# Kernel tuning notes

Hardware: AMD Instinct MI355X
Metric: run time of the kernel (lower is better)

The kernel has to match this reference:

```python
import jax, jax.numpy as jnp
import numpy as np

KH, KW, STRIDE, PAD, DIL = 3, 3, 1, 1, 1


def setup_inputs() -> dict:
    key = jax.random.key(0)
    ks = jax.random.split(key, 4)
    B, C, H, W, O = 4, 256, 64, 64, 256
    K = KH * KW
    x = jax.random.normal(ks[0], (B, C, H, W), jnp.float32)
    # offset/mask conv params (original inits to zero; use small random so offsets are non-trivial)
    w_om = jax.random.normal(ks[1], (3 * K, C, KH, KW), jnp.float32) * 0.01
    b_om = jnp.zeros((3 * K,), jnp.float32)
    # main weight: kaiming_uniform_(a=1) -> gain = sqrt(2/(1+1^2)) = 1, bound = sqrt(3)/sqrt(fan_in)
    fan_in = C * K
    bound = float(np.sqrt(3.0) / np.sqrt(fan_in))
    weight = jax.random.uniform(ks[2], (O, C, KH, KW), jnp.float32, -bound, bound)
    bias = jnp.zeros((O,), jnp.float32)
    return {"x": x, "w_om": w_om, "b_om": b_om, "weight": weight, "bias": bias}


def _deform_conv2d(x, offset, mask, weight, bias):
    # torchvision.ops.deform_conv2d semantics, deformable_groups=1, stride=1, pad=1, dil=1
    B, C, H, W = x.shape
    K = KH * KW
    # torchvision offset layout: per-tap interleaved (y, x) pairs along channel dim
    off_y = offset[:, 0::2]  # [B, K, H, W]
    off_x = offset[:, 1::2]  # [B, K, H, W]
    ky = (jnp.repeat(jnp.arange(KH), KW) * DIL).astype(x.dtype)  # [K]
    kx = (jnp.tile(jnp.arange(KW), KH) * DIL).astype(x.dtype)    # [K]
    base_y = (jnp.arange(H) * STRIDE - PAD).astype(x.dtype)
    base_x = (jnp.arange(W) * STRIDE - PAD).astype(x.dtype)
    py = base_y[None, None, :, None] + ky[None, :, None, None] + off_y  # [B,K,H,W]
    px = base_x[None, None, None, :] + kx[None, :, None, None] + off_x  # [B,K,H,W]
    y0 = jnp.floor(py)
    x0 = jnp.floor(px)
    ly = py - y0
    lx = px - x0
    y0i = y0.astype(jnp.int32)
    x0i = x0.astype(jnp.int32)
    x_flat = x.reshape(B, C, H * W)

    def gather(yy, xx):
        # zero-padded gather of one bilinear corner -> [B, C, K, H, W]
        valid = ((yy >= 0) & (yy < H) & (xx >= 0) & (xx < W)).astype(x.dtype)
        idx = (jnp.clip(yy, 0, H - 1) * W + jnp.clip(xx, 0, W - 1)).reshape(B, -1)
        g = jax.vmap(lambda xf, i: jnp.take(xf, i, axis=1))(x_flat, idx)
        return g.reshape(B, C, K, H, W) * valid.reshape(B, 1, K, H, W)

    w00 = ((1 - ly) * (1 - lx))[:, None]
    w01 = ((1 - ly) * lx)[:, None]
    w10 = (ly * (1 - lx))[:, None]
    w11 = (ly * lx)[:, None]
    val = (gather(y0i, x0i) * w00 + gather(y0i, x0i + 1) * w01
           + gather(y0i + 1, x0i) * w10 + gather(y0i + 1, x0i + 1) * w11)
    cols = val * mask[:, None]  # modulated columns [B,C,K,H,W]
    out = jnp.einsum('bckhw,ock->bohw', cols, weight.reshape(weight.shape[0], C, K))
    return out + bias[None, :, None, None]


def reference(x, w_om, b_om, weight, bias):
    om = jax.lax.conv_general_dilated(
        x, w_om, (STRIDE, STRIDE), ((PAD, PAD), (PAD, PAD)),
        rhs_dilation=(DIL, DIL), dimension_numbers=('NCHW', 'OIHW', 'NCHW'),
    ) + b_om[None, :, None, None]
    K = KH * KW
    o1, o2, m = om[:, :K], om[:, K:2 * K], om[:, 2 * K:]
    offset = jnp.concatenate([o1, o2], axis=1)  # [B, 2K, H, W]
    mask = jax.nn.sigmoid(m)                    # [B, K, H, W]
    return _deform_conv2d(x, offset, mask, weight, bias)
```

## Files before the change

kernel.cpp:

```cpp
#include <hip/hip_runtime.h>
#include <stdint.h>

#define B_ 4
#define C_ 256
#define H_ 64
#define W_ 64
#define O_ 256
#define K_ 9
#define CK 2304
#define HW 4096
#define NTOT 16384

typedef __bf16 bf16x8 __attribute__((ext_vector_type(8)));
typedef __bf16 bf16x4 __attribute__((ext_vector_type(4)));
typedef float f32x4 __attribute__((ext_vector_type(4)));
typedef float f32x2 __attribute__((ext_vector_type(2)));
typedef f32x2 __attribute__((aligned(4))) f32x2u;

__device__ __forceinline__ uint16_t f2bf(float f) {
  uint32_t u = __builtin_bit_cast(uint32_t, f);
  return (uint16_t)((u + 0x7FFFu + ((u >> 16) & 1u)) >> 16);
}

__device__ __forceinline__ uint32_t pk_bf16(float a, float b) {
  uint16_t lo = __builtin_bit_cast(uint16_t, (__bf16)a);
  uint16_t hi = __builtin_bit_cast(uint16_t, (__bf16)b);
  return (uint32_t)lo | ((uint32_t)hi << 16);
}

__global__ void kA_prep(const float* __restrict__ weight, const float* __restrict__ w_om,
                        const float* __restrict__ x, uint16_t* __restrict__ wb,
                        uint16_t* __restrict__ womb, uint16_t* __restrict__ xT) {
  int bx = blockIdx.x;
  int t = threadIdx.x;
  if (bx < 2304) {
    int idx = bx * 256 + t;
    int o = idx / CK;
    int rem = idx - o * CK;
    int k = rem >> 8, c = rem & 255;
    wb[idx] = f2bf(weight[(o * C_ + c) * K_ + k]);
  } else if (bx < 2592) {
    int idx = (bx - 2304) * 256 + t;
    int j = idx / CK;
    int ck = idx - j * CK;
    int k = ck >> 8, c = ck & 255;
    womb[idx] = (j < 27) ? f2bf(w_om[(j * 256 + c) * 9 + k]) : (uint16_t)0;
  } else {
    int bxl = bx - 2592;
    int ct = bxl & 3;
    int hwt = (bxl >> 2) & 63;
    int b = bxl >> 8;
    int l = t & 63;
    int cq = t >> 6;

    __shared__ __align__(16) uint16_t tile[64 * 72];

    const float* xb = x + ((b * 256 + ct * 64) * HW) + hwt * 64;
#pragma unroll
    for (int i = 0; i < 16; ++i) {
      int c = cq * 16 + i;
      tile[l * 72 + c] = f2bf(xb[c * HW + l]);
    }
    __syncthreads();

    int hw = t >> 2;
    int c8 = (t & 3) * 8;
    uint16_t* dst = xT + ((size_t)b << 20) + (size_t)(hwt * 64 + hw) * 256 + ct * 64;
    *(uint4*)&dst[c8] = *(const uint4*)&tile[hw * 72 + c8];
    *(uint4*)&dst[c8 + 32] = *(const uint4*)&tile[hw * 72 + c8 + 32];
  }
}

__device__ __forceinline__ void write_om(float v, int j, int n, const float* __restrict__ b_om,
                                         float* __restrict__ pypxmk) {
  if (j >= 27) return;
  float s = v + b_om[j];
  int b = n >> 12, hw = n & 4095;
  int h = hw >> 6, w = hw & 63;
  if (j < 18) {
    int k = j >> 1;
    int off = (b * 9 + k) * HW + hw;
    if ((j & 1) == 0)
      pypxmk[off] = (float)(h - 1 + k / 3) + s;
    else
      pypxmk[147456 + off] = (float)(w - 1 + k % 3) + s;
  } else {
    int k = j - 18;
    pypxmk[294912 + (b * 9 + k) * HW + hw] = 1.f / (1.f + __expf(-s));
  }
}

__global__ void k1_mfma(const uint16_t* __restrict__ womb, const uint16_t* __restrict__ xT,
                        const float* __restrict__ b_om, float* __restrict__ pypxmk) {
  int nt = blockIdx.x;
  int t = threadIdx.x;
  int lane = t & 63;
  int wid = t >> 6;
  int lr = lane & 15, q = lane >> 4;
  int n = nt * 64 + wid * 16 + lr;
  int b = n >> 12;
  int hw = n & 4095;
  int y = hw >> 6, xx = hw & 63;
  const uint16_t* xb = xT + ((size_t)b << 20);
  const uint16_t* zrow = womb + 31 * CK;

  f32x4 acc0 = {0.f, 0.f, 0.f, 0.f};
  f32x4 acc1 = {0.f, 0.f, 0.f, 0.f};

#pragma unroll
  for (int k = 0; k < 9; ++k) {
    int dy = k / 3, dx = k - dy * 3;
    int ny = y + dy - 1, nx = xx + dx - 1;
    bool valid = ((unsigned)ny < 64u) && ((unsigned)nx < 64u);
    int row = (min(max(ny, 0), 63) << 6) + min(max(nx, 0), 63);
    const uint16_t* bp = valid ? (xb + row * 256 + q * 8) : (zrow + q * 8);
    const uint16_t* ap = womb + lr * CK + k * 256 + q * 8;
#pragma unroll
    for (int kt = 0; kt < 8; ++kt) {
      int c0 = kt * 32;
      bf16x8 bF = *(const bf16x8*)&bp[c0];
      bf16x8 aF0 = *(const bf16x8*)&ap[c0];
      bf16x8 aF1 = *(const bf16x8*)&ap[16 * CK + c0];
      acc0 = __builtin_amdgcn_mfma_f32_16x16x32_bf16(aF0, bF, acc0, 0, 0, 0);
      acc1 = __builtin_amdgcn_mfma_f32_16x16x32_bf16(aF1, bF, acc1, 0, 0, 0);
    }
  }

#pragma unroll
  for (int r = 0; r < 4; ++r) {
    write_om(acc0[r], q * 4 + r, n, b_om, pypxmk);
    write_om(acc1[r], 16 + q * 4 + r, n, b_om, pypxmk);
  }
}


struct GatherState {
  float wa0[4], wb0[4], wa1[4], wb1[4];
  bf16x4 r00[4], r01[4], r10[4], r11[4];
};

__device__ __forceinline__ void gather_issue(GatherState& S, const uint16_t* __restrict__ xb,
                                             const float* __restrict__ pyA,
                                             const float* __restrict__ pxA,
                                             const float* __restrict__ mkA,
                                             int b, int kg, int n0, int rbase, int lane) {
#pragma unroll
  for (int j = 0; j < 4; ++j) {
    int nrow = rbase + j;
    int poff = (b * 9 + kg) * HW + ((n0 + nrow) & 4095);
    float py = pyA[poff];
    float px = pxA[poff];
    float mk = mkA[poff];
    float fy0 = floorf(py), fx0 = floorf(px);
    float ly = py - fy0, lx = px - fx0;
    int y0 = (int)fy0, x0 = (int)fx0;
    bool vy0 = ((unsigned)y0 < 64u), vy1 = ((unsigned)(y0 + 1) < 64u);
    bool vx0 = ((unsigned)x0 < 64u), vx1 = ((unsigned)(x0 + 1) < 64u);
    float w00 = (vy0 && vx0) ? (1.f - ly) * (1.f - lx) * mk : 0.f;
    float w01 = (vy0 && vx1) ? (1.f - ly) * lx * mk : 0.f;
    float w10 = (vy1 && vx0) ? ly * (1.f - lx) * mk : 0.f;
    float w11 = (vy1 && vx1) ? ly * lx * mk : 0.f;
    bool sel0 = (x0 >= 63);
    bool sel1 = (x0 >= 0);
    S.wa0[j] = (sel0 ? 0.f : w00) + (sel1 ? 0.f : w01);
    S.wb0[j] = (sel0 ? w00 : 0.f) + (sel1 ? w01 : 0.f);
    S.wa1[j] = (sel0 ? 0.f : w10) + (sel1 ? 0.f : w11);
    S.wb1[j] = (sel0 ? w10 : 0.f) + (sel1 ? w11 : 0.f);
    int bx0 = min(max(x0, 0), 62);
    int a0 = min(max(y0, 0), 63) * 64 + bx0;
    int a1 = min(max(y0 + 1, 0), 63) * 64 + bx0;
    S.r00[j] = *(const bf16x4*)&xb[a0 * 256 + lane * 4];
    S.r01[j] = *(const bf16x4*)&xb[a0 * 256 + 256 + lane * 4];
    S.r10[j] = *(const bf16x4*)&xb[a1 * 256 + lane * 4];
    S.r11[j] = *(const bf16x4*)&xb[a1 * 256 + 256 + lane * 4];
  }
}

__device__ __forceinline__ void gather_finish(const GatherState& S, uint16_t* bslab,
                                              int rbase, int lane) {
#pragma unroll
  for (int j = 0; j < 4; ++j) {
    int nrow = rbase + j;
    float v[4];
#pragma unroll
    for (int i = 0; i < 4; ++i)
      v[i] = S.wa0[j] * (float)S.r00[j][i] + S.wb0[j] * (float)S.r01[j][i] +
             S.wa1[j] * (float)S.r10[j][i] + S.wb1[j] * (float)S.r11[j][i];
    uint2 pk;
    pk.x = pk_bf16(v[0], v[1]);
    pk.y = pk_bf16(v[2], v[3]);
    int chunk = lane >> 1;
    int chs = (chunk & 24) | ((chunk & 7) ^ (nrow & 7));
    *(uint2*)&bslab[nrow * 256 + chs * 8 + (lane & 1) * 4] = pk;
  }
}

__device__ __forceinline__ void stageA(const uint16_t* __restrict__ wb, uint16_t* asbuf,
                                       int kbase, int t) {
#pragma unroll
  for (int i = 0; i < 4; ++i) {
    int rr = i * 64 + (t >> 3);
    const uint16_t* src = wb + rr * CK + kbase + (((t & 7) ^ (rr & 7)) << 3);
    __builtin_amdgcn_global_load_lds(
        (const __attribute__((address_space(1))) uint32_t*)src,
        (__attribute__((address_space(3))) uint32_t*)&asbuf[i * 4096 + t * 8], 16, 0, 0);
  }
}

__device__ __forceinline__ void mma_step(const uint16_t* AsP, const uint16_t* BsP,
                                         f32x4 acc[4][2], int wm, int wn, int lr, int q,
                                         int kt2) {
#pragma unroll
  for (int kc = 0; kc < 2; ++kc) {
    bf16x8 aF[4], bF[2];
#pragma unroll
    for (int i = 0; i < 4; ++i) {
      int row = wm * 64 + i * 16 + lr;
      aF[i] = *(const bf16x8*)&AsP[row * 64 + (((kc * 4 + q) ^ (row & 7)) << 3)];
    }
#pragma unroll
    for (int j = 0; j < 2; ++j) {
      int row = wn * 32 + j * 16 + lr;
      int kidx = kt2 * 8 + kc * 4 + q;
      int chs = (kidx & 24) | ((kidx & 7) ^ (row & 7));
      bF[j] = *(const bf16x8*)&BsP[row * 256 + chs * 8];
    }
#pragma unroll
    for (int i = 0; i < 4; ++i)
#pragma unroll
      for (int j = 0; j < 2; ++j)
        acc[i][j] = __builtin_amdgcn_mfma_f32_16x16x32_bf16(aF[i], bF[j], acc[i][j], 0, 0, 0);
  }
}

__global__ __launch_bounds__(512, 2) void k23_fused(const uint16_t* __restrict__ wb,
                                                    const uint16_t* __restrict__ xT,
                                                    const float* __restrict__ pypxmk,
                                                    const float* __restrict__ bias,
                                                    float* __restrict__ out) {
  __shared__ __align__(16) uint16_t As[2][16384];
  __shared__ __align__(16) uint16_t Bs[2][16384];

  int t = threadIdx.x;
  int lane = t & 63;
  int wid = __builtin_amdgcn_readfirstlane(t >> 6);
  int lr = lane & 15, q = lane >> 4;
  int wm = wid >> 1, wn = wid & 1;
  int bx = blockIdx.x;
  int swz = (bx & 7) * 32 + (bx >> 3);
  int n0 = swz * 64;
  int b = n0 >> 12;
  int hw0 = n0 & 4095;
  const uint16_t* xb = xT + ((size_t)b << 20);
  const float* pyA = pypxmk;
  const float* pxA = pypxmk + 147456;
  const float* mkA = pypxmk + 294912;

  f32x4 acc[4][2];
  const f32x4 zero = {0.f, 0.f, 0.f, 0.f};
#pragma unroll
  for (int i = 0; i < 4; ++i)
#pragma unroll
    for (int j = 0; j < 2; ++j) acc[i][j] = zero;

  GatherState S;
  int wrow = wid * 8;

  gather_issue(S, xb, pyA, pxA, mkA, b, 0, n0, wrow, lane);
  gather_finish(S, Bs[0], wrow, lane);
  gather_issue(S, xb, pyA, pxA, mkA, b, 0, n0, wrow + 4, lane);
  gather_finish(S, Bs[0], wrow + 4, lane);
  stageA(wb, As[0], 0, t);
  __syncthreads();

  for (int k = 0; k < 9; ++k) {
    uint16_t* BsC = Bs[k & 1];
    uint16_t* BsN = Bs[(k & 1) ^ 1];
    for (int kt2 = 0; kt2 < 4; ++kt2) {
      if (!(k == 8 && kt2 == 3)) {
        int kb2 = (kt2 == 3) ? (k + 1) * 256 : k * 256 + (kt2 + 1) * 64;
        stageA(wb, As[(kt2 + 1) & 1], kb2, t);
      }
      bool dogather = (k < 8) && (kt2 < 2);
      if (dogather)
        gather_issue(S, xb, pyA, pxA, mkA, b, k + 1, n0, wrow + kt2 * 4, lane);
      mma_step(As[kt2 & 1], BsC, acc, wm, wn, lr, q, kt2);
      if (dogather)
        gather_finish(S, BsN, wrow + kt2 * 4, lane);
      __syncthreads();
    }
  }

#pragma unroll
  for (int i = 0; i < 4; ++i) {
#pragma unroll
    for (int r = 0; r < 4; ++r) {
      int o = wm * 64 + i * 16 + q * 4 + r;
      float bv = bias[o];
      float* orow = out + (b * O_ + o) * HW + hw0;
#pragma unroll
      for (int j = 0; j < 2; ++j) orow[wn * 32 + j * 16 + lr] = acc[i][j][r] + bv;
    }
  }
}

__global__ void k0_wconv(const float* __restrict__ weight, uint16_t* __restrict__ wb) {
  int idx = blockIdx.x * 256 + threadIdx.x;
  if (idx >= O_ * CK) return;
  int o = idx / CK;
  int rem = idx - o * CK;
  int k = rem >> 8;
  int c = rem & 255;
  wb[idx] = f2bf(weight[(o * C_ + c) * K_ + k]);
}

__global__ void k1_offconv(const float* __restrict__ x, const float* __restrict__ w_om,
                           const float* __restrict__ b_om, float* __restrict__ pypxmk) {
  int bx = blockIdx.x;
  int jq = bx % 7;
  int h = (bx / 7) % H_;
  int b = bx / (7 * H_);
  int t = threadIdx.x;
  int w = t & 63;
  int cs = __builtin_amdgcn_readfirstlane(t >> 6);

  float acc[4] = {0.f, 0.f, 0.f, 0.f};
  const float* xb = x + (b * C_) * HW;

  for (int ci = 0; ci < 64; ++ci) {
    int c = cs * 64 + ci;
    const float* xr = xb + c * HW;
    float xv[3][3];
#pragma unroll
    for (int r = 0; r < 3; ++r) {
      int y = h - 1 + r;
      bool yv = ((unsigned)y < 64u);
#pragma unroll
      for (int dx = 0; dx < 3; ++dx) {
        int xx = w - 1 + dx;
        bool v = yv && ((unsigned)xx < 64u);
        xv[r][dx] = v ? xr[y * 64 + xx] : 0.f;
      }
    }
    const float* wp = w_om + ((jq * 4) * C_ + c) * 9;
#pragma unroll
    for (int jj = 0; jj < 4; ++jj) {
      int j = jq * 4 + jj;
      int jeff = (j < 27) ? jj : 0;
      const float* wj = wp + jeff * (C_ * 9);
      float a = 0.f;
#pragma unroll
      for (int r = 0; r < 3; ++r)
#pragma unroll
        for (int dx = 0; dx < 3; ++dx)
          a = fmaf(xv[r][dx], wj[r * 3 + dx], a);
      acc[jj] += a;
    }
  }

  __shared__ float red[4][4][64];
#pragma unroll
  for (int jj = 0; jj < 4; ++jj) red[cs][jj][w] = acc[jj];
  __syncthreads();

  int jj = t >> 6;
  int j = jq * 4 + jj;
  if (j < 27) {
    float s = red[0][jj][w] + red[1][jj][w] + red[2][jj][w] + red[3][jj][w] + b_om[j];
    float* pyA = pypxmk;
    float* pxA = pypxmk + 147456;
    float* mkA = pypxmk + 294912;
    if (j < 18) {
      int k = j >> 1;
      int off = (b * 9 + k) * HW + h * 64 + w;
      if ((j & 1) == 0)
        pyA[off] = (float)(h - 1 + k / 3) + s;
      else
        pxA[off] = (float)(w - 1 + k % 3) + s;
    } else {
      int k = j - 18;
      mkA[(b * 9 + k) * HW + h * 64 + w] = 1.f / (1.f + __expf(-s));
    }
  }
}

__global__ void k2_fb(const float* __restrict__ x, const float* __restrict__ pypxmk,
                      uint16_t* __restrict__ cols) {
  int bx = blockIdx.x;
  int cg = bx & 15;
  int h = (bx >> 4) & 63;
  int b = bx >> 10;
  int t = threadIdx.x;
  int w = t & 63;
  int g = t >> 6;

  const float* pyA = pypxmk;
  const float* pxA = pypxmk + 147456;
  const float* mkA = pypxmk + 294912;

  __shared__ uint16_t tile[64 * 146];
  const float* xb = x + b * C_ * HW;
  int cbase = cg * 16 + g * 4;

#pragma unroll
  for (int k = 0; k < 9; ++k) {
    int poff = (b * 9 + k) * HW + h * 64 + w;
    float py = pyA[poff];
    float px = pxA[poff];
    float mk = mkA[poff];
    float fy0 = floorf(py), fx0 = floorf(px);
    float ly = py - fy0, lx = px - fx0;
    int y0 = (int)fy0, x0 = (int)fx0;
    bool vy0 = ((unsigned)y0 < 64u), vy1 = ((unsigned)(y0 + 1) < 64u);
    bool vx0 = ((unsigned)x0 < 64u), vx1 = ((unsigned)(x0 + 1) < 64u);
    float w00 = (vy0 && vx0) ? (1.f - ly) * (1.f - lx) * mk : 0.f;
    float w01 = (vy0 && vx1) ? (1.f - ly) * lx * mk : 0.f;
    float w10 = (vy1 && vx0) ? ly * (1.f - lx) * mk : 0.f;
    float w11 = (vy1 && vx1) ? ly * lx * mk : 0.f;
    bool sel0 = (x0 >= 63);
    bool sel1 = (x0 >= 0);
    float wa0 = (sel0 ? 0.f : w00) + (sel1 ? 0.f : w01);
    float wb0 = (sel0 ? w00 : 0.f) + (sel1 ? w01 : 0.f);
    float wa1 = (sel0 ? 0.f : w10) + (sel1 ? 0.f : w11);
    float wb1 = (sel0 ? w10 : 0.f) + (sel1 ? w11 : 0.f);
    int bx0 = min(max(x0, 0), 62);
    int a0 = min(max(y0, 0), 63) * 64 + bx0;
    int a1 = min(max(y0 + 1, 0), 63) * 64 + bx0;

#pragma unroll
    for (int cp = 0; cp < 2; ++cp) {
      const float* xcA = xb + (cbase + cp * 2) * HW;
      const float* xcB = xcA + HW;
      f32x2 A0 = *(const f32x2u*)&xcA[a0];
      f32x2 A1 = *(const f32x2u*)&xcA[a1];
      f32x2 B0 = *(const f32x2u*)&xcB[a0];
      f32x2 B1 = *(const f32x2u*)&xcB[a1];
      float rA = wa0 * A0.x + wb0 * A0.y + wa1 * A1.x + wb1 * A1.y;
      float rB = wa0 * B0.x + wb0 * B0.y + wa1 * B1.x + wb1 * B1.y;
      *(uint32_t*)&tile[w * 146 + k * 16 + g * 4 + cp * 2] = pk_bf16(rA, rB);
    }
  }
  __syncthreads();

#pragma unroll
  for (int it = 0; it < 18; ++it) {
    int u = t + it * 256;
    int wu = u / 72;
    int rem = u - wu * 72;
    int k = rem >> 3;
    int cd = rem & 7;
    uint32_t val = *(const uint32_t*)&tile[wu * 146 + rem * 2];
    int n = b * HW + h * 64 + wu;
    int dst = n * CK + k * 256 + cg * 16 + cd * 2;
    *(uint32_t*)&cols[dst] = val;
  }
}

__global__ void k3_flex(const uint16_t* __restrict__ wb, const uint16_t* __restrict__ cols,
                        const float* __restrict__ bias, float* __restrict__ out) {
  int bx = blockIdx.x;
  int mt = bx & 1;
  int nt = bx >> 1;
  int o0 = mt * 128;
  int n0 = nt * 128;
  int t = threadIdx.x;
  int lane = t & 63;
  int wid = t >> 6;
  int wm = wid >> 1, wn = wid & 1;
  int lr = lane & 15, q = lane >> 4;

  __shared__ __align__(16) uint16_t As[128 * 32];
  __shared__ __align__(16) uint16_t Bs[128 * 32];

  f32x4 acc[4][4];
  const f32x4 zero = {0.f, 0.f, 0.f, 0.f};
#pragma unroll
  for (int i = 0; i < 4; ++i)
#pragma unroll
    for (int j = 0; j < 4; ++j) acc[i][j] = zero;

  int r0 = t >> 2;
  int koff = (t & 3) * 8;
  const uint16_t* gA = wb + (o0 + r0) * CK + koff;
  const uint16_t* gB = cols + (n0 + r0) * CK + koff;

  for (int kt = 0; kt < 72; ++kt) {
    int k0 = kt * 32;
    __builtin_amdgcn_global_load_lds(
        (const __attribute__((address_space(1))) uint32_t*)(gA + k0),
        (__attribute__((address_space(3))) uint32_t*)&As[t * 8], 16, 0, 0);
    __builtin_amdgcn_global_load_lds(
        (const __attribute__((address_space(1))) uint32_t*)(gA + 64 * CK + k0),
        (__attribute__((address_space(3))) uint32_t*)&As[2048 + t * 8], 16, 0, 0);
    __builtin_amdgcn_global_load_lds(
        (const __attribute__((address_space(1))) uint32_t*)(gB + k0),
        (__attribute__((address_space(3))) uint32_t*)&Bs[t * 8], 16, 0, 0);
    __builtin_amdgcn_global_load_lds(
        (const __attribute__((address_space(1))) uint32_t*)(gB + 64 * CK + k0),
        (__attribute__((address_space(3))) uint32_t*)&Bs[2048 + t * 8], 16, 0, 0);
    __syncthreads();

    bf16x8 aF[4], bF[4];
#pragma unroll
    for (int i = 0; i < 4; ++i)
      aF[i] = *(const bf16x8*)&As[(wm * 64 + i * 16 + lr) * 32 + q * 8];
#pragma unroll
    for (int j = 0; j < 4; ++j)
      bF[j] = *(const bf16x8*)&Bs[(wn * 64 + j * 16 + lr) * 32 + q * 8];
#pragma unroll
    for (int i = 0; i < 4; ++i)
#pragma unroll
      for (int j = 0; j < 4; ++j)
        acc[i][j] = __builtin_amdgcn_mfma_f32_16x16x32_bf16(aF[i], bF[j], acc[i][j], 0, 0, 0);
    __syncthreads();
  }

  int bb = n0 >> 12;
  int hw0 = n0 & 4095;
#pragma unroll
  for (int i = 0; i < 4; ++i) {
#pragma unroll
    for (int r = 0; r < 4; ++r) {
      int o = o0 + wm * 64 + i * 16 + q * 4 + r;
      float bv = bias[o];
      float* orow = out + (bb * O_ + o) * HW + hw0;
#pragma unroll
      for (int j = 0; j < 4; ++j) orow[wn * 64 + j * 16 + lr] = acc[i][j][r] + bv;
    }
  }
}

extern "C" void kernel_launch(void* const* d_in, const int* in_sizes, int n_in,
                              void* d_out, int out_size, void* d_ws, size_t ws_size,
                              hipStream_t stream) {
  const float* x = (const float*)d_in[0];
  const float* w_om = (const float*)d_in[1];
  const float* b_om = (const float*)d_in[2];
  const float* weight = (const float*)d_in[3];
  const float* bias = (const float*)d_in[4];
  float* out = (float*)d_out;

  char* ws = (char*)d_ws;
  uint16_t* wb = (uint16_t*)ws;
  uint16_t* womb = (uint16_t*)(ws + 1179648);
  uint16_t* xT = (uint16_t*)(ws + 1327104);
  float* pypxmk = (float*)(ws + 9715712);

  if (ws_size >= 11485184ull) {
    hipLaunchKernelGGL(kA_prep, dim3(3616), dim3(256), 0, stream, weight, w_om, x, wb, womb, xT);
    hipLaunchKernelGGL(k1_mfma, dim3(256), dim3(256), 0, stream, womb, xT, b_om, pypxmk);
    hipLaunchKernelGGL(k23_fused, dim3(256), dim3(512), 0, stream, wb, xT, pypxmk, bias, out);
  } else {
    float* pypx_fb = (float*)(ws + 1179648);
    uint16_t* colsf = (uint16_t*)(ws + 2949120);
    hipLaunchKernelGGL(k0_wconv, dim3(2304), dim3(256), 0, stream, weight, wb);
    hipLaunchKernelGGL(k1_offconv, dim3(4 * 64 * 7), dim3(256), 0, stream, x, w_om, b_om, pypx_fb);
    hipLaunchKernelGGL(k2_fb, dim3(4 * 64 * 16), dim3(256), 0, stream, x, pypx_fb, colsf);
    hipLaunchKernelGGL(k3_flex, dim3(256), dim3(256), 0, stream, wb, colsf, bias, out);
  }
}
```

Baseline: 169.6 us.

## Warp-specialize fused deform GEMM, split-K offset conv, restructure weight prep

The fused deformable-conv kernel now dedicates four waves to MFMA compute over a 256x64 tile, raising their scheduling priority, while the other four waves only do the bilinear gather for the next tap. The offset/mask conv kernel splits the 9 taps across wave groups, reduces the partial sums through shared memory, and launches twice as many blocks. Weight conversion in the prep kernel uses one block per output channel with a contiguous 9-tap read per thread. Together these aim to overlap gather latency with MMA and raise parallelism, at the cost of more accumulator registers per GEMM wave and extra LDS reduction traffic.

Measured after the change: 167.6 us. About the same (-1.2%).

```diff
diff --git a/kernel.cpp b/kernel.cpp
--- a/kernel.cpp
+++ b/kernel.cpp
@@ -33,20 +33,22 @@
                         uint16_t* __restrict__ womb, uint16_t* __restrict__ xT) {
   int bx = blockIdx.x;
   int t = threadIdx.x;
-  if (bx < 2304) {
-    int idx = bx * 256 + t;
-    int o = idx / CK;
-    int rem = idx - o * CK;
-    int k = rem >> 8, c = rem & 255;
-    wb[idx] = f2bf(weight[(o * C_ + c) * K_ + k]);
-  } else if (bx < 2592) {
-    int idx = (bx - 2304) * 256 + t;
-    int j = idx / CK;
-    int ck = idx - j * CK;
-    int k = ck >> 8, c = ck & 255;
-    womb[idx] = (j < 27) ? f2bf(w_om[(j * 256 + c) * 9 + k]) : (uint16_t)0;
+  if (bx < 256) {
+    int o = bx, c = t;
+    const float* wp = weight + (o * 256 + c) * 9;
+#pragma unroll
+    for (int k = 0; k < 9; ++k) wb[o * CK + k * 256 + c] = f2bf(wp[k]);
+  } else if (bx < 283) {
+    int j = bx - 256, c = t;
+    const float* wp = w_om + (j * 256 + c) * 9;
+#pragma unroll
+    for (int k = 0; k < 9; ++k) womb[j * CK + k * 256 + c] = f2bf(wp[k]);
+  } else if (bx < 288) {
+    int j = 27 + (bx - 283), c = t;
+#pragma unroll
+    for (int k = 0; k < 9; ++k) womb[j * CK + k * 256 + c] = 0;
   } else {
-    int bxl = bx - 2592;
+    int bxl = bx - 288;
     int ct = bxl & 3;
     int hwt = (bxl >> 2) & 63;
     int b = bxl >> 8;
@@ -90,14 +92,18 @@
   }
 }
 
-__global__ void k1_mfma(const uint16_t* __restrict__ womb, const uint16_t* __restrict__ xT,
-                        const float* __restrict__ b_om, float* __restrict__ pypxmk) {
+__global__ __launch_bounds__(512, 2) void k1_mfma(const uint16_t* __restrict__ womb,
+                                                  const uint16_t* __restrict__ xT,
+                                                  const float* __restrict__ b_om,
+                                                  float* __restrict__ pypxmk) {
   int nt = blockIdx.x;
   int t = threadIdx.x;
   int lane = t & 63;
   int wid = t >> 6;
+  int ns = wid & 1;
+  int kh = wid >> 1;
   int lr = lane & 15, q = lane >> 4;
-  int n = nt * 64 + wid * 16 + lr;
+  int n = nt * 32 + ns * 16 + lr;
   int b = n >> 12;
   int hw = n & 4095;
   int y = hw >> 6, xx = hw & 63;
@@ -107,8 +113,9 @@
   f32x4 acc0 = {0.f, 0.f, 0.f, 0.f};
   f32x4 acc1 = {0.f, 0.f, 0.f, 0.f};
 
-#pragma unroll
-  for (int k = 0; k < 9; ++k) {
+  int k0 = kh * 2;
+  int k1e = (kh == 3) ? 9 : k0 + 2;
+  for (int k = k0; k < k1e; ++k) {
     int dy = k / 3, dx = k - dy * 3;
     int ny = y + dy - 1, nx = xx + dx - 1;
     bool valid = ((unsigned)ny < 64u) && ((unsigned)nx < 64u);
@@ -126,10 +133,22 @@
     }
   }
 
+  __shared__ float red[4][2][64][8];
 #pragma unroll
   for (int r = 0; r < 4; ++r) {
-    write_om(acc0[r], q * 4 + r, n, b_om, pypxmk);
-    write_om(acc1[r], 16 + q * 4 + r, n, b_om, pypxmk);
+    red[kh][ns][lane][r] = acc0[r];
+    red[kh][ns][lane][4 + r] = acc1[r];
+  }
+  __syncthreads();
+
+  if (kh == 0) {
+#pragma unroll
+    for (int i = 0; i < 8; ++i) {
+      float s = red[0][ns][lane][i] + red[1][ns][lane][i] + red[2][ns][lane][i] +
+                red[3][ns][lane][i];
+      int j = (i < 4) ? (q * 4 + i) : (16 + q * 4 + (i - 4));
+      write_om(s, j, n, b_om, pypxmk);
+    }
   }
 }
 
@@ -195,32 +214,31 @@
   }
 }
 
-__device__ __forceinline__ void stageA(const uint16_t* __restrict__ wb, uint16_t* asbuf,
-                                       int kbase, int t) {
-#pragma unroll
-  for (int i = 0; i < 4; ++i) {
-    int rr = i * 64 + (t >> 3);
+__device__ __forceinline__ void stageA256(const uint16_t* __restrict__ wb, uint16_t* asbuf,
+                                          int kbase, int t) {
+#pragma unroll
+  for (int i = 0; i < 8; ++i) {
+    int rr = i * 32 + (t >> 3);
     const uint16_t* src = wb + rr * CK + kbase + (((t & 7) ^ (rr & 7)) << 3);
     __builtin_amdgcn_global_load_lds(
         (const __attribute__((address_space(1))) uint32_t*)src,
-        (__attribute__((address_space(3))) uint32_t*)&asbuf[i * 4096 + t * 8], 16, 0, 0);
-  }
-}
-
-__device__ __forceinline__ void mma_step(const uint16_t* AsP, const uint16_t* BsP,
-                                         f32x4 acc[4][2], int wm, int wn, int lr, int q,
-                                         int kt2) {
+        (__attribute__((address_space(3))) uint32_t*)&asbuf[i * 2048 + t * 8], 16, 0, 0);
+  }
+}
+
+__device__ __forceinline__ void mma64(const uint16_t* AsP, const uint16_t* BsP,
+                                      f32x4 acc[4][4], int wid, int lr, int q, int kt2) {
 #pragma unroll
   for (int kc = 0; kc < 2; ++kc) {
-    bf16x8 aF[4], bF[2];
+    bf16x8 aF[4], bF[4];
 #pragma unroll
     for (int i = 0; i < 4; ++i) {
-      int row = wm * 64 + i * 16 + lr;
+      int row = wid * 64 + i * 16 + lr;
       aF[i] = *(const bf16x8*)&AsP[row * 64 + (((kc * 4 + q) ^ (row & 7)) << 3)];
     }
 #pragma unroll
-    for (int j = 0; j < 2; ++j) {
-      int row = wn * 32 + j * 16 + lr;
+    for (int j = 0; j < 4; ++j) {
+      int row = j * 16 + lr;
       int kidx = kt2 * 8 + kc * 4 + q;
       int chs = (kidx & 24) | ((kidx & 7) ^ (row & 7));
       bF[j] = *(const bf16x8*)&BsP[row * 256 + chs * 8];
@@ -228,7 +246,7 @@
 #pragma unroll
     for (int i = 0; i < 4; ++i)
 #pragma unroll
-      for (int j = 0; j < 2; ++j)
+      for (int j = 0; j < 4; ++j)
         acc[i][j] = __builtin_amdgcn_mfma_f32_16x16x32_bf16(aF[i], bF[j], acc[i][j], 0, 0, 0);
   }
 }
@@ -245,7 +263,6 @@
   int lane = t & 63;
   int wid = __builtin_amdgcn_readfirstlane(t >> 6);
   int lr = lane & 15, q = lane >> 4;
-  int wm = wid >> 1, wn = wid & 1;
   int bx = blockIdx.x;
   int swz = (bx & 7) * 32 + (bx >> 3);
   int n0 = swz * 64;
@@ -256,50 +273,64 @@
   const float* pxA = pypxmk + 147456;
   const float* mkA = pypxmk + 294912;
 
-  f32x4 acc[4][2];
+  bool gemmw = (wid < 4);
+  int g = wid - 4;
+
+  f32x4 acc[4][4];
   const f32x4 zero = {0.f, 0.f, 0.f, 0.f};
 #pragma unroll
   for (int i = 0; i < 4; ++i)
 #pragma unroll
-    for (int j = 0; j < 2; ++j) acc[i][j] = zero;
+    for (int j = 0; j < 4; ++j) acc[i][j] = zero;
 
   GatherState S;
-  int wrow = wid * 8;
-
-  gather_issue(S, xb, pyA, pxA, mkA, b, 0, n0, wrow, lane);
-  gather_finish(S, Bs[0], wrow, lane);
-  gather_issue(S, xb, pyA, pxA, mkA, b, 0, n0, wrow + 4, lane);
-  gather_finish(S, Bs[0], wrow + 4, lane);
-  stageA(wb, As[0], 0, t);
+
+  if (gemmw) {
+    stageA256(wb, As[0], 0, t);
+  } else {
+#pragma unroll
+    for (int c = 0; c < 4; ++c) {
+      gather_issue(S, xb, pyA, pxA, mkA, b, 0, n0, g * 16 + c * 4, lane);
+      gather_finish(S, Bs[0], g * 16 + c * 4, lane);
+    }
+    gather_issue(S, xb, pyA, pxA, mkA, b, 1, n0, g * 16, lane);
+  }
   __syncthreads();
 
   for (int k = 0; k < 9; ++k) {
-    uint16_t* BsC = Bs[k & 1];
+    const uint16_t* BsC = Bs[k & 1];
     uint16_t* BsN = Bs[(k & 1) ^ 1];
-    for (int kt2 = 0; kt2 < 4; ++kt2) {
-      if (!(k == 8 && kt2 == 3)) {
-        int kb2 = (kt2 == 3) ? (k + 1) * 256 : k * 256 + (kt2 + 1) * 64;
-        stageA(wb, As[(kt2 + 1) & 1], kb2, t);
+    for (int s = 0; s < 4; ++s) {
+      if (gemmw) {
+        if (!(k == 8 && s == 3)) {
+          int kb = (s == 3) ? (k + 1) * 256 : k * 256 + (s + 1) * 64;
+          stageA256(wb, As[(s + 1) & 1], kb, t);
+        }
+        __builtin_amdgcn_s_setprio(1);
+        mma64(As[s & 1], BsC, acc, wid, lr, q, s);
+        __builtin_amdgcn_s_setprio(0);
+      } else if (k < 8) {
+        gather_finish(S, BsN, g * 16 + s * 4, lane);
+        if (s < 3)
+          gather_issue(S, xb, pyA, pxA, mkA, b, k + 1, n0, g * 16 + (s + 1) * 4, lane);
+        else if (k < 7)
+          gather_issue(S, xb, pyA, pxA, mkA, b, k + 2, n0, g * 16, lane);
       }
-      bool dogather = (k < 8) && (kt2 < 2);
-      if (dogather)
-        gather_issue(S, xb, pyA, pxA, mkA, b, k + 1, n0, wrow + kt2 * 4, lane);
-      mma_step(As[kt2 & 1], BsC, acc, wm, wn, lr, q, kt2);
-      if (dogather)
-        gather_finish(S, BsN, wrow + kt2 * 4, lane);
       __syncthreads();
     }
   }
 
-#pragma unroll
-  for (int i = 0; i < 4; ++i) {
-#pragma unroll
-    for (int r = 0; r < 4; ++r) {
-      int o = wm * 64 + i * 16 + q * 4 + r;
-      float bv = bias[o];
-      float* orow = out + (b * O_ + o) * HW + hw0;
-#pragma unroll
-      for (int j = 0; j < 2; ++j) orow[wn * 32 + j * 16 + lr] = acc[i][j][r] + bv;
+  if (gemmw) {
+#pragma unroll
+    for (int i = 0; i < 4; ++i) {
+#pragma unroll
+      for (int r = 0; r < 4; ++r) {
+        int o = wid * 64 + i * 16 + q * 4 + r;
+        float bv = bias[o];
+        float* orow = out + (b * O_ + o) * HW + hw0;
+#pragma unroll
+        for (int j = 0; j < 4; ++j) orow[j * 16 + lr] = acc[i][j][r] + bv;
+      }
     }
   }
 }
@@ -547,8 +578,8 @@
   float* pypxmk = (float*)(ws + 9715712);
 
   if (ws_size >= 11485184ull) {
-    hipLaunchKernelGGL(kA_prep, dim3(3616), dim3(256), 0, stream, weight, w_om, x, wb, womb, xT);
-    hipLaunchKernelGGL(k1_mfma, dim3(256), dim3(256), 0, stream, womb, xT, b_om, pypxmk);
+    hipLaunchKernelGGL(kA_prep, dim3(1312), dim3(256), 0, stream, weight, w_om, x, wb, womb, xT);
+    hipLaunchKernelGGL(k1_mfma, dim3(512), dim3(512), 0, stream, womb, xT, b_om, pypxmk);
     hipLaunchKernelGGL(k23_fused, dim3(256), dim3(512), 0, stream, wb, xT, pypxmk, bias, out);
   } else {
     float* pypx_fb = (float*)(ws + 1179648);
```
